# Performance work log

Hardware: AMD Instinct MI355X
Metric: run time of the kernel (lower is better)

## Reference

```python
import jax, jax.numpy as jnp
import numpy as np

B, T, H, W = 8, 90, 290, 180
PS = 10
NHP, NWP = H // PS, W // PS          # 29, 18
NP = NHP * NWP                        # 522 patches
PD = PS * PS                          # 100 patch dim
NV = 94                               # valid land patches
K = 24                                # visible valid patches per timestep
L = T * K                             # 2160 visible tokens per sample
D = 256
NHEAD = 8
DH = D // NHEAD
NLAYERS = 6
DFF = 4 * D
MAXT = 90


def _sinusoidal_pe(d_model, max_len):
    pos = np.arange(max_len)[:, None].astype(np.float32)
    div = np.exp(np.arange(0, d_model, 2).astype(np.float32) * (-np.log(10000.0) / d_model))
    pe = np.zeros((max_len, d_model), np.float32)
    pe[:, 0::2] = np.sin(pos * div)
    pe[:, 1::2] = np.cos(pos * div)
    return jnp.asarray(pe)


def _layernorm(x, s, b, eps=1e-5):
    m = x.mean(-1, keepdims=True)
    v = ((x - m) ** 2).mean(-1, keepdims=True)
    return (x - m) * jax.lax.rsqrt(v + eps) * s + b


def setup_inputs():
    key = jax.random.key(0)
    ks = jax.random.split(key, 12)
    x_img = jax.random.normal(ks[0], (B, T, H, W), jnp.float32)
    valid_idx = jnp.sort(jax.random.choice(ks[1], NP, (NV,), replace=False)).astype(jnp.int32)
    # patch_mask: True = masked. Exactly K visible among the NV valid patches per (b, t).
    scores = jax.random.uniform(ks[2], (B, T, NV))
    vis = jnp.argsort(scores, axis=-1)[..., :K]  # [B,T,K] indices into valid set
    mask_valid = jnp.ones((B, T, NV), bool).at[
        jnp.arange(B)[:, None, None], jnp.arange(T)[None, :, None], vis].set(False)
    patch_mask = jnp.ones((B, T, NP), bool).at[:, :, valid_idx].set(mask_valid)

    def init(k, shape, fan):
        return jax.random.normal(k, shape, jnp.float32) / np.sqrt(fan)

    return {
        "x_img": x_img,
        "patch_mask": patch_mask,
        "valid_idx": valid_idx,
        "patch_embed_w": init(ks[3], (D, PD), PD),
        "patch_embed_b": jnp.zeros((D,), jnp.float32),
        "spatial_pos": 0.02 * jax.random.normal(ks[4], (NV, D), jnp.float32),
        "Wqkv": init(ks[5], (NLAYERS, 3 * D, D), D),
        "bqkv": jnp.zeros((NLAYERS, 3 * D), jnp.float32),
        "Wo": init(ks[6], (NLAYERS, D, D), D),
        "bo": jnp.zeros((NLAYERS, D), jnp.float32),
        "ln1_s": jnp.ones((NLAYERS, D), jnp.float32),
        "ln1_b": jnp.zeros((NLAYERS, D), jnp.float32),
        "W1": init(ks[7], (NLAYERS, DFF, D), D),
        "b1": jnp.zeros((NLAYERS, DFF), jnp.float32),
        "W2": init(ks[8], (NLAYERS, D, DFF), DFF),
        "b2": jnp.zeros((NLAYERS, D), jnp.float32),
        "ln2_s": jnp.ones((NLAYERS, D), jnp.float32),
        "ln2_b": jnp.zeros((NLAYERS, D), jnp.float32),
        "normf_s": jnp.ones((D,), jnp.float32),
        "normf_b": jnp.zeros((D,), jnp.float32),
    }


def reference(x_img, patch_mask, valid_idx, patch_embed_w, patch_embed_b, spatial_pos,
              Wqkv, bqkv, Wo, bo, ln1_s, ln1_b, W1, b1, W2, b2, ln2_s, ln2_b,
              normf_s, normf_b):
    # 1) patchify: [B,T,H,W] -> [B,T,NP,PD]
    p = x_img.reshape(B, T, NHP, PS, NWP, PS).transpose(0, 1, 2, 4, 3, 5).reshape(B, T, NP, PD)
    p = p[:, :, valid_idx, :]                          # [B,T,NV,PD]
    mv = patch_mask[:, :, valid_idx]                   # True = masked
    flat = p.reshape(B, T * NV, PD)
    mflat = mv.reshape(B, T * NV)
    # 2) stable compaction: visible (False) tokens first, preserving (t, patch) order
    order = jnp.argsort(mflat.astype(jnp.int32), axis=1)[:, :L]   # jnp.argsort is stable
    bidx = jnp.arange(B)[:, None]
    x = flat[bidx, order]                              # [B,L,PD]
    lengths = (~mflat).sum(1)                          # [B]
    pad = jnp.arange(L)[None, :] >= lengths[:, None]   # [B,L] True = padding
    x = jnp.where(pad[..., None], 0.0, x)
    t_idx = order // NV                                # time index of each token
    p_idx = order % NV                                 # valid-patch index of each token
    # 3) embed + positional encodings
    x = x @ patch_embed_w.T + patch_embed_b            # [B,L,D]
    pe = _sinusoidal_pe(D, MAXT)
    x = x + jnp.where(pad[..., None], 0.0, spatial_pos[p_idx] + pe[t_idx])
    # 4) transformer encoder (PyTorch post-norm, relu FFN)
    neg = jnp.where(pad, -1e9, 0.0)[:, None, None, :]  # [B,1,1,L]
    scale = 1.0 / np.sqrt(DH)
    for i in range(NLAYERS):
        qkv = x @ Wqkv[i].T + bqkv[i]
        q, k, v = jnp.split(qkv, 3, axis=-1)
        q = q.reshape(B, L, NHEAD, DH)
        k = k.reshape(B, L, NHEAD, DH)
        v = v.reshape(B, L, NHEAD, DH)
        s = jnp.einsum('bqhd,bkhd->bhqk', q, k) * scale + neg
        a = jax.nn.softmax(s, axis=-1)
        o = jnp.einsum('bhqk,bkhd->bqhd', a, v).reshape(B, L, D)
        o = o @ Wo[i].T + bo[i]
        x = _layernorm(x + o, ln1_s[i], ln1_b[i])
        f = jax.nn.relu(x @ W1[i].T + b1[i]) @ W2[i].T + b2[i]
        x = _layernorm(x + f, ln2_s[i], ln2_b[i])
    # 5) final norm; output is the visible-token sequence [B,L,D]
    return _layernorm(x, normf_s, normf_b)
```

## Files before the change

### kernel.cpp

```cpp
#include <hip/hip_runtime.h>
#include <hip/hip_bf16.h>
#include <math.h>

#define BB 8
#define TT 90
#define HH 290
#define WWI 180
#define PSZ 10
#define NHPc 29
#define NWPc 18
#define NPc 522
#define PDc 100
#define NVc 94
#define KKc 24
#define LLc 2160
#define LPc 2176
#define DDc 256
#define NHEADc 8
#define DHc 32
#define NLc 6
#define DFFc 1024
#define MTOT (BB*LLc)

using f32x4 = __attribute__((ext_vector_type(4))) float;
using s16x8 = __attribute__((ext_vector_type(8))) short;
using s16x4 = __attribute__((ext_vector_type(4))) short;

__device__ __forceinline__ short f2bf(float f) {
  union { __hip_bfloat16 h; short s; } u;
  u.h = __float2bfloat16(f);
  return u.s;
}

__global__ void cvt_bf16_kernel(const float* __restrict__ src, short* __restrict__ dst, int n) {
  int i = blockIdx.x * 256 + threadIdx.x;
  if (i < n) dst[i] = f2bf(src[i]);
}

__global__ void pe_kernel(float* __restrict__ pe) {
  int idx = blockIdx.x * 256 + threadIdx.x;
  if (idx >= TT * 128) return;
  int t = idx / 128, i = idx % 128;
  float div = expf((2.0f * i) * (-9.210340371976184f / 256.0f));
  float ang = (float)t * div;
  pe[t * DDc + 2 * i]     = sinf(ang);
  pe[t * DDc + 2 * i + 1] = cosf(ang);
}

__global__ void order_kernel(const unsigned char* __restrict__ pm8,
                             const int* __restrict__ vidx, int* __restrict__ pidx) {
  int gw = (blockIdx.x * blockDim.x + threadIdx.x) >> 6;
  int lane = threadIdx.x & 63;
  if (gw >= BB * TT) return;
  size_t base = (size_t)gw * NPc;
  int v0 = lane, v1 = 64 + lane;
  bool vis0 = (pm8[base + vidx[v0]] == 0);
  bool vis1 = (v1 < NVc) && (pm8[base + vidx[v1]] == 0);
  unsigned long long b0 = __ballot(vis0), b1 = __ballot(vis1);
  if (__popcll(b0) + __popcll(b1) != KKc) {
    const int* pm32 = (const int*)pm8;
    vis0 = (pm32[base + vidx[v0]] == 0);
    vis1 = (v1 < NVc) && (pm32[base + vidx[v1]] == 0);
    b0 = __ballot(vis0); b1 = __ballot(vis1);
  }
  int* outp = pidx + gw * KKc;
  unsigned long long lt = (1ull << lane) - 1ull;
  if (vis0) outp[__popcll(b0 & lt)] = v0;
  if (vis1) outp[__popcll(b0) + __popcll(b1 & lt)] = v1;
}

__global__ __launch_bounds__(256) void embed_kernel(
    const float* __restrict__ ximg, const int* __restrict__ vidx,
    const int* __restrict__ pidx, const float* __restrict__ pew,
    const float* __restrict__ peb, const float* __restrict__ sp,
    const float* __restrict__ petab, float* __restrict__ x, short* __restrict__ xb) {
  __shared__ float px[4][PDc];
  int m0 = blockIdx.x * 4;
  for (int idx = threadIdx.x; idx < 4 * PDc; idx += 256) {
    int tok = idx / PDc, k = idx % PDc;
    int m = m0 + tok;
    int b = m / LLc, l = m % LLc;
    int t = l / KKc;
    int v = pidx[m];
    int np_ = vidx[v];
    int hp = np_ / NWPc, wp = np_ % NWPc;
    int r = k / PSZ, c = k % PSZ;
    px[tok][k] = ximg[(((size_t)b * TT + t) * HH + hp * PSZ + r) * WWI + wp * PSZ + c];
  }
  __syncthreads();
  int d = threadIdx.x;
  float a0 = 0.f, a1 = 0.f, a2 = 0.f, a3 = 0.f;
  const float* wrow = pew + (size_t)d * PDc;
#pragma unroll 4
  for (int k = 0; k < PDc; k++) {
    float w = wrow[k];
    a0 += w * px[0][k]; a1 += w * px[1][k]; a2 += w * px[2][k]; a3 += w * px[3][k];
  }
  float accs[4] = {a0, a1, a2, a3};
#pragma unroll
  for (int tok = 0; tok < 4; tok++) {
    int m = m0 + tok;
    int l = m % LLc; int t = l / KKc;
    int v = pidx[m];
    float val = accs[tok] + peb[d] + sp[(size_t)v * DDc + d] + petab[(size_t)t * DDc + d];
    x[(size_t)m * DDc + d] = val;
    xb[(size_t)m * DDc + d] = f2bf(val);
  }
}

#define GM_QKV 0
#define GM_F32 1
#define GM_RELU 2

template <int MODE>
__global__ __launch_bounds__(256) void gemm_bt(
    const short* __restrict__ A, int lda,
    const short* __restrict__ W, int ldw,
    const float* __restrict__ bias,
    void* __restrict__ outp, int N, int K,
    short* __restrict__ vT, float qscale) {
  __shared__ short As[64][40];
  __shared__ short Ws[64][40];
  int tid = threadIdx.x;
  int m0 = blockIdx.x * 64;
  int n0 = blockIdx.y * 64;
  int wave = tid >> 6, lane = tid & 63;
  int wr = (wave >> 1) * 32, wc = (wave & 1) * 32;
  int g = lane >> 4, c = lane & 15;
  f32x4 acc[2][2];
#pragma unroll
  for (int i = 0; i < 2; i++)
#pragma unroll
    for (int j = 0; j < 2; j++) { acc[i][j][0] = 0.f; acc[i][j][1] = 0.f; acc[i][j][2] = 0.f; acc[i][j][3] = 0.f; }
  int lrow = tid >> 2, lcg = (tid & 3) * 8;
  const short* aptr = A + (size_t)(m0 + lrow) * lda + lcg;
  const short* wptr = W + (size_t)(n0 + lrow) * ldw + lcg;
  for (int k0 = 0; k0 < K; k0 += 32) {
    *(s16x8*)&As[lrow][lcg] = *(const s16x8*)(aptr + k0);
    *(s16x8*)&Ws[lrow][lcg] = *(const s16x8*)(wptr + k0);
    __syncthreads();
    s16x8 va0 = *(const s16x8*)&As[wr + c][g * 8];
    s16x8 va1 = *(const s16x8*)&As[wr + 16 + c][g * 8];
    s16x8 vb0 = *(const s16x8*)&Ws[wc + c][g * 8];
    s16x8 vb1 = *(const s16x8*)&Ws[wc + 16 + c][g * 8];
    acc[0][0] = __builtin_amdgcn_mfma_f32_16x16x32_bf16(va0, vb0, acc[0][0], 0, 0, 0);
    acc[0][1] = __builtin_amdgcn_mfma_f32_16x16x32_bf16(va0, vb1, acc[0][1], 0, 0, 0);
    acc[1][0] = __builtin_amdgcn_mfma_f32_16x16x32_bf16(va1, vb0, acc[1][0], 0, 0, 0);
    acc[1][1] = __builtin_amdgcn_mfma_f32_16x16x32_bf16(va1, vb1, acc[1][1], 0, 0, 0);
    __syncthreads();
  }
#pragma unroll
  for (int i = 0; i < 2; i++)
#pragma unroll
    for (int j = 0; j < 2; j++) {
      int mbase = m0 + wr + i * 16 + g * 4;
      int n = n0 + wc + j * 16 + c;
      float bv = bias[n];
#pragma unroll
      for (int r = 0; r < 4; r++) {
        int m = mbase + r;
        float val = acc[i][j][r] + bv;
        if (MODE == GM_QKV) {
          int b = m / LLc, l = m % LLc;
          if (n < 512) {
            if (n < 256) val *= qscale;
            ((short*)outp)[((size_t)b * LPc + l) * 768 + n] = f2bf(val);
          } else {
            vT[((size_t)b * DDc + (n - 512)) * LPc + l] = f2bf(val);
          }
        } else if (MODE == GM_F32) {
          ((float*)outp)[(size_t)m * N + n] = val;
        } else {
          ((short*)outp)[(size_t)m * N + n] = f2bf(val > 0.f ? val : 0.f);
        }
      }
    }
}

__device__ __forceinline__ void flash_body(
    int kt, const short* kbase, const short* vbase_cg, short* pw,
    const s16x8& qfA, const s16x8& qfB, const s16x8& ones,
    s16x8& K0, s16x8& K1, s16x8& V0, s16x8& V1,
    f32x4& o0a, f32x4& o1a, f32x4& osa,
    f32x4& o0b, f32x4& o1b, f32x4& osb, int g, int c) {
  s16x8 ck0 = K0, ck1 = K1, cv0 = V0, cv1 = V1;
  int nk = kt * 32 + 64;
  if (nk >= LPc) nk = 0;
  K0 = *(const s16x8*)(kbase + (size_t)(nk + c) * 768);
  K1 = *(const s16x8*)(kbase + (size_t)(nk + 16 + c) * 768);
  V0 = *(const s16x8*)(vbase_cg + nk);
  V1 = *(const s16x8*)(vbase_cg + nk + 16 * LPc);
  f32x4 zero4; zero4[0] = zero4[1] = zero4[2] = zero4[3] = 0.f;
  f32x4 s0a = __builtin_amdgcn_mfma_f32_16x16x32_bf16(qfA, ck0, zero4, 0, 0, 0);
  f32x4 s1a = __builtin_amdgcn_mfma_f32_16x16x32_bf16(qfA, ck1, zero4, 0, 0, 0);
  f32x4 s0b = __builtin_amdgcn_mfma_f32_16x16x32_bf16(qfB, ck0, zero4, 0, 0, 0);
  f32x4 s1b = __builtin_amdgcn_mfma_f32_16x16x32_bf16(qfB, ck1, zero4, 0, 0, 0);
  if (kt == 67) {
    s1a[0] = s1a[1] = s1a[2] = s1a[3] = -1e30f;
    s1b[0] = s1b[1] = s1b[2] = s1b[3] = -1e30f;
  }
#pragma unroll
  for (int i = 0; i < 4; i++) {
    pw[(g * 4 + i) * 40 + c]           = f2bf(exp2f(s0a[i]));
    pw[(g * 4 + i) * 40 + 16 + c]      = f2bf(exp2f(s1a[i]));
    pw[(16 + g * 4 + i) * 40 + c]      = f2bf(exp2f(s0b[i]));
    pw[(16 + g * 4 + i) * 40 + 16 + c] = f2bf(exp2f(s1b[i]));
  }
  s16x8 pa0 = *(const s16x8*)(pw + c * 40 + g * 8);
  s16x8 pa1 = *(const s16x8*)(pw + (16 + c) * 40 + g * 8);
  o0a = __builtin_amdgcn_mfma_f32_16x16x32_bf16(pa0, cv0, o0a, 0, 0, 0);
  o1a = __builtin_amdgcn_mfma_f32_16x16x32_bf16(pa0, cv1, o1a, 0, 0, 0);
  osa = __builtin_amdgcn_mfma_f32_16x16x32_bf16(pa0, ones, osa, 0, 0, 0);
  o0b = __builtin_amdgcn_mfma_f32_16x16x32_bf16(pa1, cv0, o0b, 0, 0, 0);
  o1b = __builtin_amdgcn_mfma_f32_16x16x32_bf16(pa1, cv1, o1b, 0, 0, 0);
  osb = __builtin_amdgcn_mfma_f32_16x16x32_bf16(pa1, ones, osb, 0, 0, 0);
}

__global__ __launch_bounds__(256) void flash_kernel(
    const short* __restrict__ qkv, const short* __restrict__ vT,
    short* __restrict__ attnout) {
  __shared__ short plds[4][2][32 * 40];
  int wave = threadIdx.x >> 6, lane = threadIdx.x & 63;
  int g = lane >> 4, c = lane & 15;
  int bh = blockIdx.y;
  int b = bh >> 3, h = bh & 7;
  int q0 = blockIdx.x * 128 + wave * 32;

  const short* qbase = qkv + ((size_t)b * LPc + q0 + c) * 768 + h * 32 + g * 8;
  s16x8 qfA = *(const s16x8*)qbase;
  s16x8 qfB = *(const s16x8*)(qbase + 16 * 768);
  const short* kbase = qkv + (size_t)b * LPc * 768 + 256 + h * 32 + g * 8;
  const short* vbase_cg = vT + ((size_t)b * DDc + h * 32 + c) * LPc + g * 8;
  short* pw0 = &plds[wave][0][0];
  short* pw1 = &plds[wave][1][0];

  f32x4 o0a, o1a, osa, o0b, o1b, osb;
  o0a[0]=o0a[1]=o0a[2]=o0a[3]=0.f; o1a[0]=o1a[1]=o1a[2]=o1a[3]=0.f;
  osa[0]=osa[1]=osa[2]=osa[3]=0.f; o0b[0]=o0b[1]=o0b[2]=o0b[3]=0.f;
  o1b[0]=o1b[1]=o1b[2]=o1b[3]=0.f; osb[0]=osb[1]=osb[2]=osb[3]=0.f;
  s16x8 ones;
#pragma unroll
  for (int j = 0; j < 8; j++) ones[j] = (short)0x3F80;

  s16x8 kA0 = *(const s16x8*)(kbase + (size_t)(0 + c) * 768);
  s16x8 kA1 = *(const s16x8*)(kbase + (size_t)(16 + c) * 768);
  s16x8 vA0 = *(const s16x8*)(vbase_cg + 0);
  s16x8 vA1 = *(const s16x8*)(vbase_cg + 16 * LPc);
  s16x8 kB0 = *(const s16x8*)(kbase + (size_t)(32 + c) * 768);
  s16x8 kB1 = *(const s16x8*)(kbase + (size_t)(48 + c) * 768);
  s16x8 vB0 = *(const s16x8*)(vbase_cg + 32);
  s16x8 vB1 = *(const s16x8*)(vbase_cg + 32 + 16 * LPc);

  for (int kt = 0; kt < 68; kt += 2) {
    flash_body(kt,     kbase, vbase_cg, pw0, qfA, qfB, ones,
               kA0, kA1, vA0, vA1, o0a, o1a, osa, o0b, o1b, osb, g, c);
    flash_body(kt + 1, kbase, vbase_cg, pw1, qfA, qfB, ones,
               kB0, kB1, vB0, vB1, o0a, o1a, osa, o0b, o1b, osb, g, c);
  }
#pragma unroll
  for (int i = 0; i < 4; i++) {
    int la = q0 + g * 4 + i;
    if (la < LLc) {
      float inv = 1.0f / osa[i];
      attnout[((size_t)b * LLc + la) * DDc + h * 32 + c]      = f2bf(o0a[i] * inv);
      attnout[((size_t)b * LLc + la) * DDc + h * 32 + 16 + c] = f2bf(o1a[i] * inv);
    }
    int lb = q0 + 16 + g * 4 + i;
    if (lb < LLc) {
      float inv = 1.0f / osb[i];
      attnout[((size_t)b * LLc + lb) * DDc + h * 32 + c]      = f2bf(o0b[i] * inv);
      attnout[((size_t)b * LLc + lb) * DDc + h * 32 + 16 + c] = f2bf(o1b[i] * inv);
    }
  }
}

__global__ __launch_bounds__(256) void ln_kernel(
    const float* __restrict__ xin, const float* __restrict__ res,
    const float* __restrict__ gs, const float* __restrict__ gb,
    float* __restrict__ xout, short* __restrict__ xbout, int rows) {
  int wid = (blockIdx.x * 256 + threadIdx.x) >> 6;
  int lane = threadIdx.x & 63;
  if (wid >= rows) return;
  int dbase = lane * 4;
  float4 v = *(const float4*)(xin + (size_t)wid * DDc + dbase);
  if (res) {
    float4 r = *(const float4*)(res + (size_t)wid * DDc + dbase);
    v.x += r.x; v.y += r.y; v.z += r.z; v.w += r.w;
  }
  float s = v.x + v.y + v.z + v.w;
#pragma unroll
  for (int d = 1; d < 64; d <<= 1) s += __shfl_xor(s, d);
  float mean = s * (1.0f / 256.0f);
  float dx = v.x - mean, dy = v.y - mean, dz = v.z - mean, dw = v.w - mean;
  float sq = dx * dx + dy * dy + dz * dz + dw * dw;
#pragma unroll
  for (int d = 1; d < 64; d <<= 1) sq += __shfl_xor(sq, d);
  float rstd = rsqrtf(sq * (1.0f / 256.0f) + 1e-5f);
  float4 sg = *(const float4*)(gs + dbase);
  float4 bg = *(const float4*)(gb + dbase);
  float o0 = dx * rstd * sg.x + bg.x;
  float o1 = dy * rstd * sg.y + bg.y;
  float o2 = dz * rstd * sg.z + bg.z;
  float o3 = dw * rstd * sg.w + bg.w;
  float4 ov; ov.x = o0; ov.y = o1; ov.z = o2; ov.w = o3;
  *(float4*)(xout + (size_t)wid * DDc + dbase) = ov;
  if (xbout) {
    s16x4 pb;
    pb[0] = f2bf(o0); pb[1] = f2bf(o1); pb[2] = f2bf(o2); pb[3] = f2bf(o3);
    *(s16x4*)(xbout + (size_t)wid * DDc + dbase) = pb;
  }
}

extern "C" void kernel_launch(void* const* d_in, const int* in_sizes, int n_in,
                              void* d_out, int out_size, void* d_ws, size_t ws_size,
                              hipStream_t stream) {
  const float* x_img = (const float*)d_in[0];
  const unsigned char* pmask = (const unsigned char*)d_in[1];
  const int* vidx = (const int*)d_in[2];
  const float* pew = (const float*)d_in[3];
  const float* peb = (const float*)d_in[4];
  const float* sp = (const float*)d_in[5];
  const float* Wqkv = (const float*)d_in[6];
  const float* bqkv = (const float*)d_in[7];
  const float* Wo = (const float*)d_in[8];
  const float* bo = (const float*)d_in[9];
  const float* ln1s = (const float*)d_in[10];
  const float* ln1b = (const float*)d_in[11];
  const float* W1 = (const float*)d_in[12];
  const float* b1 = (const float*)d_in[13];
  const float* W2 = (const float*)d_in[14];
  const float* b2 = (const float*)d_in[15];
  const float* ln2s = (const float*)d_in[16];
  const float* ln2b = (const float*)d_in[17];
  const float* nfs = (const float*)d_in[18];
  const float* nfb = (const float*)d_in[19];

  char* ws = (char*)d_ws;
  size_t o_wq = 0;
  size_t o_wo = o_wq + (size_t)NLc * 768 * DDc * 2;
  size_t o_w1 = o_wo + (size_t)NLc * DDc * DDc * 2;
  size_t o_w2 = o_w1 + (size_t)NLc * DFFc * DDc * 2;
  size_t o_pe = o_w2 + (size_t)NLc * DFFc * DDc * 2;
  size_t o_pi = o_pe + (size_t)TT * DDc * 4;
  size_t o_x  = o_pi + (size_t)MTOT * 4;
  size_t o_xb = o_x  + (size_t)MTOT * DDc * 4;
  size_t o_qk = o_xb + (size_t)MTOT * DDc * 2;
  size_t o_vt = o_qk + (size_t)BB * LPc * 768 * 2;
  size_t o_at = o_vt + (size_t)BB * DDc * LPc * 2;
  size_t o_h  = o_at + (size_t)MTOT * DDc * 2;
  size_t o_ob = o_qk;

  short* wqb = (short*)(ws + o_wq);
  short* wob = (short*)(ws + o_wo);
  short* w1b = (short*)(ws + o_w1);
  short* w2b = (short*)(ws + o_w2);
  float* petab = (float*)(ws + o_pe);
  int* pidx = (int*)(ws + o_pi);
  float* xbuf = (float*)(ws + o_x);
  short* xb = (short*)(ws + o_xb);
  short* qkvb = (short*)(ws + o_qk);
  short* vtb = (short*)(ws + o_vt);
  short* atb = (short*)(ws + o_at);
  short* hb = (short*)(ws + o_h);
  float* obuf = (float*)(ws + o_ob);

  const float qscale = 0.17677669529663687f * 1.4426950408889634f;

  {
    int n;
    n = NLc * 768 * DDc;  cvt_bf16_kernel<<<(n + 255) / 256, 256, 0, stream>>>(Wqkv, wqb, n);
    n = NLc * DDc * DDc;  cvt_bf16_kernel<<<(n + 255) / 256, 256, 0, stream>>>(Wo, wob, n);
    n = NLc * DFFc * DDc; cvt_bf16_kernel<<<(n + 255) / 256, 256, 0, stream>>>(W1, w1b, n);
    n = NLc * DFFc * DDc; cvt_bf16_kernel<<<(n + 255) / 256, 256, 0, stream>>>(W2, w2b, n);
  }
  pe_kernel<<<(TT * 128 + 255) / 256, 256, 0, stream>>>(petab);
  order_kernel<<<(BB * TT + 3) / 4, 256, 0, stream>>>(pmask, vidx, pidx);
  embed_kernel<<<MTOT / 4, 256, 0, stream>>>(x_img, vidx, pidx, pew, peb, sp, petab, xbuf, xb);

  for (int i = 0; i < NLc; i++) {
    gemm_bt<GM_QKV><<<dim3(MTOT / 64, 768 / 64), 256, 0, stream>>>(
        xb, DDc, wqb + (size_t)i * 768 * DDc, DDc, bqkv + i * 768,
        qkvb, 768, DDc, vtb, qscale);
    flash_kernel<<<dim3(LPc / 128, BB * NHEADc), 256, 0, stream>>>(qkvb, vtb, atb);
    gemm_bt<GM_F32><<<dim3(MTOT / 64, DDc / 64), 256, 0, stream>>>(
        atb, DDc, wob + (size_t)i * DDc * DDc, DDc, bo + i * DDc,
        obuf, DDc, DDc, nullptr, 0.f);
    ln_kernel<<<MTOT / 4, 256, 0, stream>>>(xbuf, obuf, ln1s + i * DDc, ln1b + i * DDc, xbuf, xb, MTOT);
    gemm_bt<GM_RELU><<<dim3(MTOT / 64, DFFc / 64), 256, 0, stream>>>(
        xb, DDc, w1b + (size_t)i * DFFc * DDc, DDc, b1 + i * DFFc,
        hb, DFFc, DDc, nullptr, 0.f);
    gemm_bt<GM_F32><<<dim3(MTOT / 64, DDc / 64), 256, 0, stream>>>(
        hb, DFFc, w2b + (size_t)i * DFFc * DDc, DFFc, b2 + i * DDc,
        obuf, DDc, DFFc, nullptr, 0.f);
    ln_kernel<<<MTOT / 4, 256, 0, stream>>>(xbuf, obuf, ln2s + i * DDc, ln2b + i * DDc, xbuf, xb, MTOT);
  }
  ln_kernel<<<MTOT / 4, 256, 0, stream>>>(xbuf, nullptr, nfs, nfb, (float*)d_out, nullptr, MTOT);
}
```

Before: 2.123 ms.

## Enlarge GEMM tiles to 128xBN and load via global_load_lds

Replaces the 64x64 GEMM with a templated 128-row kernel that uses 128x128 or 128x64 tiles, so each wave computes a 64xWN sub-tile with more MFMAs per shared-memory load. Global-to-LDS copies now use the direct global_load_lds builtin instead of staging through registers. The aim is better operand reuse and less load-instruction and register overhead in the projection and FFN GEMMs. In exchange, the grid has fewer blocks and the LDS tiles lose the padding that previously avoided bank conflicts. MTOT (17280) divides evenly by 128, so no bounds checks are needed.

```diff
diff --git a/kernel.cpp b/kernel.cpp
--- a/kernel.cpp
+++ b/kernel.cpp
@@ -32,6 +32,12 @@
   return u.s;
 }
 
+__device__ __forceinline__ void gload16(const short* g, short* l) {
+  __builtin_amdgcn_global_load_lds(
+      (const __attribute__((address_space(1))) void*)g,
+      (__attribute__((address_space(3))) void*)l, 16, 0, 0);
+}
+
 __global__ void cvt_bf16_kernel(const float* __restrict__ src, short* __restrict__ dst, int n) {
   int i = blockIdx.x * 256 + threadIdx.x;
   if (i < n) dst[i] = f2bf(src[i]);
@@ -112,50 +118,69 @@
 #define GM_F32 1
 #define GM_RELU 2
 
-template <int MODE>
-__global__ __launch_bounds__(256) void gemm_bt(
+template <int MODE, int BN>
+__global__ __launch_bounds__(256) void gemm128(
     const short* __restrict__ A, int lda,
     const short* __restrict__ W, int ldw,
     const float* __restrict__ bias,
     void* __restrict__ outp, int N, int K,
     short* __restrict__ vT, float qscale) {
-  __shared__ short As[64][40];
-  __shared__ short Ws[64][40];
+  constexpr int WN = BN / 2;
+  constexpr int NF = WN / 16;
+  __shared__ short As[128 * 32];
+  __shared__ short Bs[BN * 32];
   int tid = threadIdx.x;
-  int m0 = blockIdx.x * 64;
-  int n0 = blockIdx.y * 64;
   int wave = tid >> 6, lane = tid & 63;
-  int wr = (wave >> 1) * 32, wc = (wave & 1) * 32;
   int g = lane >> 4, c = lane & 15;
-  f32x4 acc[2][2];
-#pragma unroll
-  for (int i = 0; i < 2; i++)
-#pragma unroll
-    for (int j = 0; j < 2; j++) { acc[i][j][0] = 0.f; acc[i][j][1] = 0.f; acc[i][j][2] = 0.f; acc[i][j][3] = 0.f; }
-  int lrow = tid >> 2, lcg = (tid & 3) * 8;
-  const short* aptr = A + (size_t)(m0 + lrow) * lda + lcg;
-  const short* wptr = W + (size_t)(n0 + lrow) * ldw + lcg;
+  int m0 = blockIdx.x * 128, n0 = blockIdx.y * BN;
+  int wr = (wave >> 1) * 64, wc = (wave & 1) * WN;
+
+  int lr = lane >> 2;
+  int scol = (lane & 3) * 8;
+  const short* asrc = A + (size_t)(m0 + wave * 32 + lr) * lda + scol;
+  short* aldst = As + wave * 1024;
+  const short* wsrc;
+  short* bldst;
+  if (BN == 128) {
+    wsrc = W + (size_t)(n0 + wave * 32 + lr) * ldw + scol;
+    bldst = Bs + wave * 1024;
+  } else {
+    wsrc = W + (size_t)(n0 + wave * 16 + lr) * ldw + scol;
+    bldst = Bs + wave * 512;
+  }
+
+  f32x4 acc[4][NF];
+#pragma unroll
+  for (int i = 0; i < 4; i++)
+#pragma unroll
+    for (int j = 0; j < NF; j++) { acc[i][j][0]=0.f; acc[i][j][1]=0.f; acc[i][j][2]=0.f; acc[i][j][3]=0.f; }
+
   for (int k0 = 0; k0 < K; k0 += 32) {
-    *(s16x8*)&As[lrow][lcg] = *(const s16x8*)(aptr + k0);
-    *(s16x8*)&Ws[lrow][lcg] = *(const s16x8*)(wptr + k0);
+    gload16(asrc + k0, aldst);
+    gload16(asrc + 16 * lda + k0, aldst + 512);
+    gload16(wsrc + k0, bldst);
+    if (BN == 128) gload16(wsrc + 16 * ldw + k0, bldst + 512);
     __syncthreads();
-    s16x8 va0 = *(const s16x8*)&As[wr + c][g * 8];
-    s16x8 va1 = *(const s16x8*)&As[wr + 16 + c][g * 8];
-    s16x8 vb0 = *(const s16x8*)&Ws[wc + c][g * 8];
-    s16x8 vb1 = *(const s16x8*)&Ws[wc + 16 + c][g * 8];
-    acc[0][0] = __builtin_amdgcn_mfma_f32_16x16x32_bf16(va0, vb0, acc[0][0], 0, 0, 0);
-    acc[0][1] = __builtin_amdgcn_mfma_f32_16x16x32_bf16(va0, vb1, acc[0][1], 0, 0, 0);
-    acc[1][0] = __builtin_amdgcn_mfma_f32_16x16x32_bf16(va1, vb0, acc[1][0], 0, 0, 0);
-    acc[1][1] = __builtin_amdgcn_mfma_f32_16x16x32_bf16(va1, vb1, acc[1][1], 0, 0, 0);
+    s16x8 af[4], bf[NF];
+#pragma unroll
+    for (int f = 0; f < 4; f++) af[f] = *(const s16x8*)&As[(wr + f * 16 + c) * 32 + g * 8];
+#pragma unroll
+    for (int f = 0; f < NF; f++) bf[f] = *(const s16x8*)&Bs[(wc + f * 16 + c) * 32 + g * 8];
+#pragma unroll
+    for (int i = 0; i < 4; i++)
+#pragma unroll
+      for (int j = 0; j < NF; j++)
+        acc[i][j] = __builtin_amdgcn_mfma_f32_16x16x32_bf16(af[i], bf[j], acc[i][j], 0, 0, 0);
     __syncthreads();
   }
-#pragma unroll
-  for (int i = 0; i < 2; i++)
-#pragma unroll
-    for (int j = 0; j < 2; j++) {
-      int mbase = m0 + wr + i * 16 + g * 4;
+
+#pragma unroll
+  for (int i = 0; i < 4; i++) {
+#pragma unroll
+    for (int j = 0; j < NF; j++) {
       int n = n0 + wc + j * 16 + c;
       float bv = bias[n];
+      int mbase = m0 + wr + i * 16 + g * 4;
 #pragma unroll
       for (int r = 0; r < 4; r++) {
         int m = mbase + r;
@@ -175,6 +200,7 @@
         }
       }
     }
+  }
 }
 
 __device__ __forceinline__ void flash_body(
@@ -378,18 +404,18 @@
   embed_kernel<<<MTOT / 4, 256, 0, stream>>>(x_img, vidx, pidx, pew, peb, sp, petab, xbuf, xb);
 
   for (int i = 0; i < NLc; i++) {
-    gemm_bt<GM_QKV><<<dim3(MTOT / 64, 768 / 64), 256, 0, stream>>>(
+    gemm128<GM_QKV, 128><<<dim3(MTOT / 128, 768 / 128), 256, 0, stream>>>(
         xb, DDc, wqb + (size_t)i * 768 * DDc, DDc, bqkv + i * 768,
         qkvb, 768, DDc, vtb, qscale);
     flash_kernel<<<dim3(LPc / 128, BB * NHEADc), 256, 0, stream>>>(qkvb, vtb, atb);
-    gemm_bt<GM_F32><<<dim3(MTOT / 64, DDc / 64), 256, 0, stream>>>(
+    gemm128<GM_F32, 64><<<dim3(MTOT / 128, DDc / 64), 256, 0, stream>>>(
         atb, DDc, wob + (size_t)i * DDc * DDc, DDc, bo + i * DDc,
         obuf, DDc, DDc, nullptr, 0.f);
     ln_kernel<<<MTOT / 4, 256, 0, stream>>>(xbuf, obuf, ln1s + i * DDc, ln1b + i * DDc, xbuf, xb, MTOT);
-    gemm_bt<GM_RELU><<<dim3(MTOT / 64, DFFc / 64), 256, 0, stream>>>(
+    gemm128<GM_RELU, 128><<<dim3(MTOT / 128, DFFc / 128), 256, 0, stream>>>(
         xb, DDc, w1b + (size_t)i * DFFc * DDc, DDc, b1 + i * DFFc,
         hb, DFFc, DDc, nullptr, 0.f);
-    gemm_bt<GM_F32><<<dim3(MTOT / 64, DDc / 64), 256, 0, stream>>>(
+    gemm128<GM_F32, 64><<<dim3(MTOT / 128, DDc / 64), 256, 0, stream>>>(
         hb, DFFc, w2b + (size_t)i * DFFc * DDc, DFFc, b2 + i * DDc,
         obuf, DDc, DFFc, nullptr, 0.f);
     ln_kernel<<<MTOT / 4, 256, 0, stream>>>(xbuf, obuf, ln2s + i * DDc, ln2b + i * DDc, xbuf, xb, MTOT);
```

Measured after the change: 2.108 ms. About the same (-0.7%).
